# Performance work log

Measured on AMD Instinct MI355X. Metric: run time of the kernel, lower is better.

## Reference

```python
import jax, jax.numpy as jnp
import numpy as np

N_NODES = 50000
N_EDGES = 400000
D = 64        # hidden_features
H_NE = 16     # hidden_ne_features
L = 4         # num_layers
EPS = 1e-5


def _ln(z, g, b):
    # layer norm over feature dim
    mu = jnp.mean(z, axis=-1, keepdims=True)
    var = jnp.var(z, axis=-1, keepdims=True)
    return (z - mu) * jax.lax.rsqrt(var + EPS) * g + b


def setup_inputs() -> dict:
    key = jax.random.key(0)
    ks = iter(jax.random.split(key, 64))
    def rn(shape, s=0.05):
        return jax.random.normal(next(ks), shape, dtype=jnp.float32) * s
    inp = {
        "x": rn((N_NODES, 2), 1.0),
        "e": rn((N_EDGES, 2), 1.0),
        "src": jax.random.randint(next(ks), (N_EDGES,), 0, N_NODES, dtype=jnp.int32),
        "dst": jax.random.randint(next(ks), (N_EDGES,), 0, N_NODES, dtype=jnp.int32),
        # node / edge encoders (2-layer MLPs)
        "ne_W1": rn((2, H_NE)), "ne_b1": jnp.zeros((H_NE,), jnp.float32),
        "ne_W2": rn((H_NE, D)), "ne_b2": jnp.zeros((D,), jnp.float32),
        "ee_W1": rn((2, H_NE)), "ee_b1": jnp.zeros((H_NE,), jnp.float32),
        "ee_W2": rn((H_NE, D)), "ee_b2": jnp.zeros((D,), jnp.float32),
        # stacked per-layer GatedGCN weights
        "A1": rn((L, D, D)), "bA1": jnp.zeros((L, D), jnp.float32),
        "A2": rn((L, D, D)), "bA2": jnp.zeros((L, D), jnp.float32),
        "A3": rn((L, D, D)), "bA3": jnp.zeros((L, D), jnp.float32),
        "B1": rn((L, D, D)), "bB1": jnp.zeros((L, D), jnp.float32),
        "B2": rn((L, D, D)), "bB2": jnp.zeros((L, D), jnp.float32),
        "B3": rn((L, D, D)), "bB3": jnp.zeros((L, D), jnp.float32),
        "ge": jnp.ones((L, D), jnp.float32), "be": jnp.zeros((L, D), jnp.float32),
        "gh": jnp.ones((L, D), jnp.float32), "bh": jnp.zeros((L, D), jnp.float32),
        # score predictor
        "pW1": rn((3 * D, D)), "pb1": jnp.zeros((D,), jnp.float32),
        "pW2": rn((D, 1)), "pb2": jnp.zeros((1,), jnp.float32),
    }
    return inp


def _forward(x, e, src, dst,
             ne_W1, ne_b1, ne_W2, ne_b2,
             ee_W1, ee_b1, ee_W2, ee_b2,
             A1, bA1, A2, bA2, A3, bA3,
             B1, bB1, B2, bB2, B3, bB3,
             ge, be, gh, bh,
             pW1, pb1, pW2, pb2):
    # encoders
    x = jax.nn.relu(x @ ne_W1 + ne_b1) @ ne_W2 + ne_b2      # [N, D]
    e = jax.nn.relu(e @ ee_W1 + ee_b1) @ ee_W2 + ee_b2      # [E, D]

    params = {"A1": A1, "bA1": bA1, "A2": A2, "bA2": bA2,
              "A3": A3, "bA3": bA3, "B1": B1, "bB1": bB1,
              "B2": B2, "bB2": bB2, "B3": B3, "bB3": bB3,
              "ge": ge, "be": be, "gh": gh, "bh": bh}

    def layer(carry, p):
        x, e = carry
        # edge update: e_ij += ReLU(LN(B1 h_i + B2 h_j + B3 e_ij))
        e_hat = (x[src] @ p["B1"] + p["bB1"]
                 + x[dst] @ p["B2"] + p["bB2"]
                 + e @ p["B3"] + p["bB3"])                  # [E, D]
        e = e + jax.nn.relu(_ln(e_hat, p["ge"], p["be"]))
        sigma = jax.nn.sigmoid(e)                             # gates [E, D]
        # directed aggregation: forward (src->dst) and backward (dst->src)
        a2 = x @ p["A2"] + p["bA2"]
        a3 = x @ p["A3"] + p["bA3"]
        m_f = jax.ops.segment_sum(sigma * a2[src], dst, num_segments=N_NODES)
        d_f = jax.ops.segment_sum(sigma, dst, num_segments=N_NODES)
        m_b = jax.ops.segment_sum(sigma * a3[dst], src, num_segments=N_NODES)
        d_b = jax.ops.segment_sum(sigma, src, num_segments=N_NODES)
        h = (x @ p["A1"] + p["bA1"]
             + m_f / (d_f + EPS) + m_b / (d_b + EPS))        # [N, D]
        x = x + jax.nn.relu(_ln(h, p["gh"], p["bh"]))
        return (x, e), None

    (x, e), _ = jax.lax.scan(layer, (x, e), params)

    # score predictor: MLP over cat(x_src, x_dst, e)
    z = jnp.concatenate([x[src], x[dst], e], axis=-1)        # [E, 3D]
    return jax.nn.relu(z @ pW1 + pb1) @ pW2 + pb2            # [E, 1]


def reference(x, e, src, dst,
              ne_W1, ne_b1, ne_W2, ne_b2,
              ee_W1, ee_b1, ee_W2, ee_b2,
              A1, bA1, A2, bA2, A3, bA3,
              B1, bB1, B2, bB2, B3, bB3,
              ge, be, gh, bh,
              pW1, pb1, pW2, pb2):
    return _forward(x, e, src, dst,
                    ne_W1, ne_b1, ne_W2, ne_b2,
                    ee_W1, ee_b1, ee_W2, ee_b2,
                    A1, bA1, A2, bA2, A3, bA3,
                    B1, bB1, B2, bB2, B3, bB3,
                    ge, be, gh, bh,
                    pW1, pb1, pW2, pb2)
```

## Files before the change

kernel.cpp:

```cpp
#include <hip/hip_runtime.h>

#define N_NODES 50000
#define N_EDGES 400000
#define EPSV 1e-5f

__global__ __launch_bounds__(256) void encode_kernel(
    const float* __restrict__ in2, const float* __restrict__ W1,
    const float* __restrict__ b1, const float* __restrict__ W2,
    const float* __restrict__ b2, float* __restrict__ out, int nrows)
{
  int t = blockIdx.x * 256 + threadIdx.x;
  int row = t >> 4;
  int d0 = t & 15;
  if (row >= nrows) return;
  float x0 = in2[row * 2 + 0], x1 = in2[row * 2 + 1];
  float h[16];
#pragma unroll
  for (int j = 0; j < 16; ++j)
    h[j] = fmaxf(fmaf(x0, W1[j], fmaf(x1, W1[16 + j], b1[j])), 0.f);
#pragma unroll
  for (int q = 0; q < 4; ++q) {
    int d = d0 + q * 16;
    float a = b2[d];
#pragma unroll
    for (int j = 0; j < 16; ++j) a = fmaf(h[j], W2[j * 64 + d], a);
    out[(size_t)row * 64 + d] = a;
  }
}

__global__ __launch_bounds__(256) void hist_kernel(
    const int* __restrict__ src, const int* __restrict__ dst,
    int* __restrict__ cnt_f, int* __restrict__ cnt_b)
{
  int t = blockIdx.x * 256 + threadIdx.x;
  if (t >= N_EDGES) return;
  atomicAdd(&cnt_f[dst[t]], 1);
  atomicAdd(&cnt_b[src[t]], 1);
}

__global__ __launch_bounds__(1024) void scan_kernel(
    const int* __restrict__ cnt_f, const int* __restrict__ cnt_b,
    int* __restrict__ off_f, int* __restrict__ off_b,
    int* __restrict__ cur_f, int* __restrict__ cur_b)
{
  __shared__ int sh[1024];
  const int n = N_NODES;
  const int SEG = (n + 1023) / 1024;
  const int* cnt = blockIdx.x ? cnt_b : cnt_f;
  int* off = blockIdx.x ? off_b : off_f;
  int* cur = blockIdx.x ? cur_b : cur_f;
  int t = threadIdx.x;
  int base = t * SEG;
  int s = 0;
  for (int i = 0; i < SEG; ++i) {
    int idx = base + i;
    if (idx < n) s += cnt[idx];
  }
  sh[t] = s;
  __syncthreads();
  for (int o = 1; o < 1024; o <<= 1) {
    int v = sh[t];
    int u = (t >= o) ? sh[t - o] : 0;
    __syncthreads();
    sh[t] = v + u;
    __syncthreads();
  }
  int run = (t > 0) ? sh[t - 1] : 0;
  for (int i = 0; i < SEG; ++i) {
    int idx = base + i;
    if (idx < n) {
      off[idx] = run;
      cur[idx] = run;
      run += cnt[idx];
    }
  }
  if (t == 1023) off[n] = sh[1023];
}

__global__ __launch_bounds__(256) void fill_kernel(
    const int* __restrict__ src, const int* __restrict__ dst,
    int* __restrict__ cur_f, int* __restrict__ cur_b,
    int2* __restrict__ csr_f, int2* __restrict__ csr_b)
{
  int t = blockIdx.x * 256 + threadIdx.x;
  if (t >= N_EDGES) return;
  int dv = dst[t], sv = src[t];
  int p = atomicAdd(&cur_f[dv], 1);
  csr_f[p] = make_int2(t, sv);
  int q = atomicAdd(&cur_b[sv], 1);
  csr_b[q] = make_int2(t, dv);
}

__global__ __launch_bounds__(256) void sort_kernel(
    const int* __restrict__ off_f, const int* __restrict__ off_b,
    int2* __restrict__ csr_f, int2* __restrict__ csr_b)
{
  int t = blockIdx.x * 256 + threadIdx.x;
  int n;
  int2* csr;
  const int* off;
  if (t < N_NODES) { n = t; csr = csr_f; off = off_f; }
  else if (t < 2 * N_NODES) { n = t - N_NODES; csr = csr_b; off = off_b; }
  else return;
  int b = off[n], e = off[n + 1];
  for (int i = b + 1; i < e; ++i) {
    int2 key = csr[i];
    int j = i - 1;
    while (j >= b && csr[j].x > key.x) { csr[j + 1] = csr[j]; --j; }
    csr[j + 1] = key;
  }
}


__global__ __launch_bounds__(256, 3) void node_gemm_kernel(
    const float* __restrict__ X,
    const float* __restrict__ A1, const float* __restrict__ A2,
    const float* __restrict__ A3, const float* __restrict__ B1,
    const float* __restrict__ B2,
    const float* __restrict__ bA1, const float* __restrict__ bA2,
    const float* __restrict__ bA3, const float* __restrict__ bB1,
    const float* __restrict__ bB2,
    float* __restrict__ NA, int l)
{
  __shared__ float ett[4][64 * 36];
  const int NT = 1563;
  int wid = threadIdx.x >> 6;
  int lane = threadIdx.x & 63;
  int wf = blockIdx.x * 4 + wid;
  if (wf >= 5 * NT) return;
  int m = wf / NT;
  int t = wf - m * NT;
  int row0 = t * 32;
  int r8 = lane & 7, c8 = lane >> 3;
  int col = 8 * c8;
  float* tl = ett[wid];
#pragma unroll
  for (int rb = 0; rb < 8; ++rb) {
    int r = row0 + 4 * rb;
    float v0 = (r + 0 < N_NODES) ? X[(size_t)(r + 0) * 64 + lane] : 0.f;
    float v1 = (r + 1 < N_NODES) ? X[(size_t)(r + 1) * 64 + lane] : 0.f;
    float v2 = (r + 2 < N_NODES) ? X[(size_t)(r + 2) * 64 + lane] : 0.f;
    float v3 = (r + 3 < N_NODES) ? X[(size_t)(r + 3) * 64 + lane] : 0.f;
    *reinterpret_cast<float4*>(&tl[lane * 36 + 4 * rb]) =
        make_float4(v0, v1, v2, v3);
  }
  const float* W;
  const float* bb;
  if (m == 0) { W = A1; bb = bA1; }
  else if (m == 1) { W = A2; bb = bA2; }
  else if (m == 2) { W = A3; bb = bA3; }
  else if (m == 3) { W = B1; bb = bB1; }
  else { W = B2; bb = bB2; }
  W += l * 64 * 64;
  float acc[4][8];
#pragma unroll
  for (int i = 0; i < 4; ++i)
#pragma unroll
    for (int j = 0; j < 8; ++j) acc[i][j] = 0.f;
#pragma unroll 8
  for (int k = 0; k < 64; ++k) {
    float4 er = *reinterpret_cast<const float4*>(&tl[k * 36 + 4 * r8]);
    float4 w0 = *reinterpret_cast<const float4*>(&W[k * 64 + col]);
    float4 w1 = *reinterpret_cast<const float4*>(&W[k * 64 + col + 4]);
    float ev[4] = {er.x, er.y, er.z, er.w};
    float wv[8] = {w0.x, w0.y, w0.z, w0.w, w1.x, w1.y, w1.z, w1.w};
#pragma unroll
    for (int i = 0; i < 4; ++i)
#pragma unroll
      for (int j = 0; j < 8; ++j) acc[i][j] = fmaf(ev[i], wv[j], acc[i][j]);
  }
  float4 b0 = *reinterpret_cast<const float4*>(&bb[l * 64 + col]);
  float4 b1 = *reinterpret_cast<const float4*>(&bb[l * 64 + col + 4]);
  float* out = NA + (size_t)m * N_NODES * 64;
#pragma unroll
  for (int i = 0; i < 4; ++i) {
    int row = row0 + 4 * r8 + i;
    if (row < N_NODES) {
      *reinterpret_cast<float4*>(&out[(size_t)row * 64 + col]) =
          make_float4(acc[i][0] + b0.x, acc[i][1] + b0.y, acc[i][2] + b0.z,
                      acc[i][3] + b0.w);
      *reinterpret_cast<float4*>(&out[(size_t)row * 64 + col + 4]) =
          make_float4(acc[i][4] + b1.x, acc[i][5] + b1.y, acc[i][6] + b1.z,
                      acc[i][7] + b1.w);
    }
  }
}

__global__ __launch_bounds__(256, 3) void edge_update_kernel(
    const float* __restrict__ NA,
    const float* __restrict__ B3, const float* __restrict__ bB3,
    const float* __restrict__ ge, const float* __restrict__ be,
    const int* __restrict__ src, const int* __restrict__ dst,
    float* __restrict__ E64, int l)
{
  __shared__ float ett[4][64 * 36];
  int wid = threadIdx.x >> 6;
  int lane = threadIdx.x & 63;
  int tile = blockIdx.x * 4 + wid;
  int e0 = tile * 32;
  int r8 = lane & 7, c8 = lane >> 3;
  int col = 8 * c8;
  float* tl = ett[wid];
#pragma unroll
  for (int rb = 0; rb < 8; ++rb) {
    int r = e0 + 4 * rb;
    float v0 = E64[(size_t)(r + 0) * 64 + lane];
    float v1 = E64[(size_t)(r + 1) * 64 + lane];
    float v2 = E64[(size_t)(r + 2) * 64 + lane];
    float v3 = E64[(size_t)(r + 3) * 64 + lane];
    *reinterpret_cast<float4*>(&tl[lane * 36 + 4 * rb]) =
        make_float4(v0, v1, v2, v3);
  }
  const float* W = B3 + l * 64 * 64;
  float acc[4][8];
#pragma unroll
  for (int i = 0; i < 4; ++i)
#pragma unroll
    for (int j = 0; j < 8; ++j) acc[i][j] = 0.f;
#pragma unroll 8
  for (int k = 0; k < 64; ++k) {
    float4 er = *reinterpret_cast<const float4*>(&tl[k * 36 + 4 * r8]);
    float4 w0 = *reinterpret_cast<const float4*>(&W[k * 64 + col]);
    float4 w1 = *reinterpret_cast<const float4*>(&W[k * 64 + col + 4]);
    float ev[4] = {er.x, er.y, er.z, er.w};
    float wv[8] = {w0.x, w0.y, w0.z, w0.w, w1.x, w1.y, w1.z, w1.w};
#pragma unroll
    for (int i = 0; i < 4; ++i)
#pragma unroll
      for (int j = 0; j < 8; ++j) acc[i][j] = fmaf(ev[i], wv[j], acc[i][j]);
  }
  const float* b1x = NA + (size_t)3 * N_NODES * 64;
  const float* b2x = NA + (size_t)4 * N_NODES * 64;
  float4 t0, t1;
  t0 = *reinterpret_cast<const float4*>(&bB3[l * 64 + col]);
  t1 = *reinterpret_cast<const float4*>(&bB3[l * 64 + col + 4]);
  float bbv[8] = {t0.x, t0.y, t0.z, t0.w, t1.x, t1.y, t1.z, t1.w};
  t0 = *reinterpret_cast<const float4*>(&ge[l * 64 + col]);
  t1 = *reinterpret_cast<const float4*>(&ge[l * 64 + col + 4]);
  float gev[8] = {t0.x, t0.y, t0.z, t0.w, t1.x, t1.y, t1.z, t1.w};
  t0 = *reinterpret_cast<const float4*>(&be[l * 64 + col]);
  t1 = *reinterpret_cast<const float4*>(&be[l * 64 + col + 4]);
  float bev[8] = {t0.x, t0.y, t0.z, t0.w, t1.x, t1.y, t1.z, t1.w};
#pragma unroll
  for (int i = 0; i < 4; ++i) {
    int row = e0 + 4 * r8 + i;
    int sv = src[row], dv = dst[row];
    float4 g0 = *reinterpret_cast<const float4*>(&b1x[(size_t)sv * 64 + col]);
    float4 g1 = *reinterpret_cast<const float4*>(&b1x[(size_t)sv * 64 + col + 4]);
    float4 h0 = *reinterpret_cast<const float4*>(&b2x[(size_t)dv * 64 + col]);
    float4 h1 = *reinterpret_cast<const float4*>(&b2x[(size_t)dv * 64 + col + 4]);
    float4 o0 = *reinterpret_cast<const float4*>(&E64[(size_t)row * 64 + col]);
    float4 o1 = *reinterpret_cast<const float4*>(&E64[(size_t)row * 64 + col + 4]);
    float g1v[8] = {g0.x, g0.y, g0.z, g0.w, g1.x, g1.y, g1.z, g1.w};
    float g2v[8] = {h0.x, h0.y, h0.z, h0.w, h1.x, h1.y, h1.z, h1.w};
    float eov[8] = {o0.x, o0.y, o0.z, o0.w, o1.x, o1.y, o1.z, o1.w};
    float z[8];
    float s1 = 0.f, s2 = 0.f;
#pragma unroll
    for (int j = 0; j < 8; ++j) {
      z[j] = acc[i][j] + bbv[j] + g1v[j] + g2v[j];
      s1 += z[j];
      s2 = fmaf(z[j], z[j], s2);
    }
    s1 += __shfl_xor(s1, 8, 64);  s2 += __shfl_xor(s2, 8, 64);
    s1 += __shfl_xor(s1, 16, 64); s2 += __shfl_xor(s2, 16, 64);
    s1 += __shfl_xor(s1, 32, 64); s2 += __shfl_xor(s2, 32, 64);
    float mean = s1 * (1.f / 64.f);
    float var = fmaxf(s2 * (1.f / 64.f) - mean * mean, 0.f);
    float rstd = rsqrtf(var + EPSV);
    float o[8];
#pragma unroll
    for (int j = 0; j < 8; ++j)
      o[j] = eov[j] + fmaxf(fmaf((z[j] - mean) * rstd, gev[j], bev[j]), 0.f);
    *reinterpret_cast<float4*>(&E64[(size_t)row * 64 + col]) =
        make_float4(o[0], o[1], o[2], o[3]);
    *reinterpret_cast<float4*>(&E64[(size_t)row * 64 + col + 4]) =
        make_float4(o[4], o[5], o[6], o[7]);
  }
}

__global__ __launch_bounds__(256) void aggregate_kernel(
    const float* __restrict__ NA, const float* __restrict__ E64,
    const int* __restrict__ off_f, const int* __restrict__ off_b,
    const int2* __restrict__ csr_f, const int2* __restrict__ csr_b,
    const float* __restrict__ gh, const float* __restrict__ bh,
    float* __restrict__ X, int l)
{
  int wave = threadIdx.x >> 6;
  int lane = threadIdx.x & 63;
  int n = blockIdx.x * 4 + wave;
  if (n >= N_NODES) return;
  const float* A1x = NA;
  const float* A2x = NA + (size_t)N_NODES * 64;
  const float* A3x = NA + (size_t)2 * N_NODES * 64;
  float xo = X[(size_t)n * 64 + lane];
  float a1v = A1x[(size_t)n * 64 + lane];
  float ghv = gh[l * 64 + lane];
  float bhv = bh[l * 64 + lane];
  int pf = off_f[n], pfe = off_f[n + 1];
  int pb = off_b[n], pbe = off_b[n + 1];
  float mf = 0.f, df = 0.f, mb = 0.f, db = 0.f;
  bool hf = pf < pfe, hb = pb < pbe;
  float evf = 0.f, avf = 0.f, evb = 0.f, avb = 0.f;
  if (hf) {
    int2 c = csr_f[pf];
    evf = E64[(size_t)c.x * 64 + lane];
    avf = A2x[(size_t)c.y * 64 + lane];
  }
  if (hb) {
    int2 c = csr_b[pb];
    evb = E64[(size_t)c.x * 64 + lane];
    avb = A3x[(size_t)c.y * 64 + lane];
  }
  while (hf || hb) {
    bool nf = (pf + 1) < pfe;
    bool nb = (pb + 1) < pbe;
    float evf2 = 0.f, avf2 = 0.f, evb2 = 0.f, avb2 = 0.f;
    if (nf) {
      int2 c = csr_f[pf + 1];
      evf2 = E64[(size_t)c.x * 64 + lane];
      avf2 = A2x[(size_t)c.y * 64 + lane];
    }
    if (nb) {
      int2 c = csr_b[pb + 1];
      evb2 = E64[(size_t)c.x * 64 + lane];
      avb2 = A3x[(size_t)c.y * 64 + lane];
    }
    if (hf) {
      float sg = __builtin_amdgcn_rcpf(1.f + __expf(-evf));
      mf = fmaf(sg, avf, mf);
      df += sg;
      ++pf;
      evf = evf2;
      avf = avf2;
      hf = nf;
    }
    if (hb) {
      float sg = __builtin_amdgcn_rcpf(1.f + __expf(-evb));
      mb = fmaf(sg, avb, mb);
      db += sg;
      ++pb;
      evb = evb2;
      avb = avb2;
      hb = nb;
    }
  }
  float h = a1v + mf * __builtin_amdgcn_rcpf(df + EPSV) +
            mb * __builtin_amdgcn_rcpf(db + EPSV);
  float s1 = h, s2 = h * h;
#pragma unroll
  for (int m = 1; m < 64; m <<= 1) {
    s1 += __shfl_xor(s1, m, 64);
    s2 += __shfl_xor(s2, m, 64);
  }
  float mean = s1 * (1.f / 64.f);
  float var = fmaxf(s2 * (1.f / 64.f) - mean * mean, 0.f);
  float rstd = rsqrtf(var + EPSV);
  X[(size_t)n * 64 + lane] =
      xo + fmaxf(fmaf((h - mean) * rstd, ghv, bhv), 0.f);
}

__global__ __launch_bounds__(256, 3) void pred_node_kernel(
    const float* __restrict__ X, const float* __restrict__ pW1,
    float* __restrict__ U, float* __restrict__ V)
{
  __shared__ float ett[4][64 * 36];
  const int NT = 1563;
  int wid = threadIdx.x >> 6;
  int lane = threadIdx.x & 63;
  int wf = blockIdx.x * 4 + wid;
  if (wf >= 2 * NT) return;
  int m = wf / NT;
  int t = wf - m * NT;
  int row0 = t * 32;
  int r8 = lane & 7, c8 = lane >> 3;
  int col = 8 * c8;
  float* tl = ett[wid];
#pragma unroll
  for (int rb = 0; rb < 8; ++rb) {
    int r = row0 + 4 * rb;
    float v0 = (r + 0 < N_NODES) ? X[(size_t)(r + 0) * 64 + lane] : 0.f;
    float v1 = (r + 1 < N_NODES) ? X[(size_t)(r + 1) * 64 + lane] : 0.f;
    float v2 = (r + 2 < N_NODES) ? X[(size_t)(r + 2) * 64 + lane] : 0.f;
    float v3 = (r + 3 < N_NODES) ? X[(size_t)(r + 3) * 64 + lane] : 0.f;
    *reinterpret_cast<float4*>(&tl[lane * 36 + 4 * rb]) =
        make_float4(v0, v1, v2, v3);
  }
  const float* W = pW1 + (size_t)m * 64 * 64;
  float acc[4][8];
#pragma unroll
  for (int i = 0; i < 4; ++i)
#pragma unroll
    for (int j = 0; j < 8; ++j) acc[i][j] = 0.f;
#pragma unroll 8
  for (int k = 0; k < 64; ++k) {
    float4 er = *reinterpret_cast<const float4*>(&tl[k * 36 + 4 * r8]);
    float4 w0 = *reinterpret_cast<const float4*>(&W[k * 64 + col]);
    float4 w1 = *reinterpret_cast<const float4*>(&W[k * 64 + col + 4]);
    float ev[4] = {er.x, er.y, er.z, er.w};
    float wv[8] = {w0.x, w0.y, w0.z, w0.w, w1.x, w1.y, w1.z, w1.w};
#pragma unroll
    for (int i = 0; i < 4; ++i)
#pragma unroll
      for (int j = 0; j < 8; ++j) acc[i][j] = fmaf(ev[i], wv[j], acc[i][j]);
  }
  float* out = m ? V : U;
#pragma unroll
  for (int i = 0; i < 4; ++i) {
    int row = row0 + 4 * r8 + i;
    if (row < N_NODES) {
      *reinterpret_cast<float4*>(&out[(size_t)row * 64 + col]) =
          make_float4(acc[i][0], acc[i][1], acc[i][2], acc[i][3]);
      *reinterpret_cast<float4*>(&out[(size_t)row * 64 + col + 4]) =
          make_float4(acc[i][4], acc[i][5], acc[i][6], acc[i][7]);
    }
  }
}

__global__ __launch_bounds__(256, 3) void pred_edge_kernel(
    const float* __restrict__ U, const float* __restrict__ V,
    const float* __restrict__ E64,
    const int* __restrict__ src, const int* __restrict__ dst,
    const float* __restrict__ pW1, const float* __restrict__ pb1,
    const float* __restrict__ pW2, const float* __restrict__ pb2,
    float* __restrict__ out)
{
  __shared__ float ett[4][64 * 36];
  int wid = threadIdx.x >> 6;
  int lane = threadIdx.x & 63;
  int tile = blockIdx.x * 4 + wid;
  int e0 = tile * 32;
  int r8 = lane & 7, c8 = lane >> 3;
  int col = 8 * c8;
  float* tl = ett[wid];
#pragma unroll
  for (int rb = 0; rb < 8; ++rb) {
    int r = e0 + 4 * rb;
    float v0 = E64[(size_t)(r + 0) * 64 + lane];
    float v1 = E64[(size_t)(r + 1) * 64 + lane];
    float v2 = E64[(size_t)(r + 2) * 64 + lane];
    float v3 = E64[(size_t)(r + 3) * 64 + lane];
    *reinterpret_cast<float4*>(&tl[lane * 36 + 4 * rb]) =
        make_float4(v0, v1, v2, v3);
  }
  const float* W = pW1 + (size_t)128 * 64;
  float acc[4][8];
#pragma unroll
  for (int i = 0; i < 4; ++i)
#pragma unroll
    for (int j = 0; j < 8; ++j) acc[i][j] = 0.f;
#pragma unroll 8
  for (int k = 0; k < 64; ++k) {
    float4 er = *reinterpret_cast<const float4*>(&tl[k * 36 + 4 * r8]);
    float4 w0 = *reinterpret_cast<const float4*>(&W[k * 64 + col]);
    float4 w1 = *reinterpret_cast<const float4*>(&W[k * 64 + col + 4]);
    float ev[4] = {er.x, er.y, er.z, er.w};
    float wv[8] = {w0.x, w0.y, w0.z, w0.w, w1.x, w1.y, w1.z, w1.w};
#pragma unroll
    for (int i = 0; i < 4; ++i)
#pragma unroll
      for (int j = 0; j < 8; ++j) acc[i][j] = fmaf(ev[i], wv[j], acc[i][j]);
  }
  float4 t0, t1;
  t0 = *reinterpret_cast<const float4*>(&pb1[col]);
  t1 = *reinterpret_cast<const float4*>(&pb1[col + 4]);
  float pb1v[8] = {t0.x, t0.y, t0.z, t0.w, t1.x, t1.y, t1.z, t1.w};
  t0 = *reinterpret_cast<const float4*>(&pW2[col]);
  t1 = *reinterpret_cast<const float4*>(&pW2[col + 4]);
  float pw2v[8] = {t0.x, t0.y, t0.z, t0.w, t1.x, t1.y, t1.z, t1.w};
  float pb2v = pb2[0];
#pragma unroll
  for (int i = 0; i < 4; ++i) {
    int row = e0 + 4 * r8 + i;
    int sv = src[row], dv = dst[row];
    float4 g0 = *reinterpret_cast<const float4*>(&U[(size_t)sv * 64 + col]);
    float4 g1 = *reinterpret_cast<const float4*>(&U[(size_t)sv * 64 + col + 4]);
    float4 h0 = *reinterpret_cast<const float4*>(&V[(size_t)dv * 64 + col]);
    float4 h1 = *reinterpret_cast<const float4*>(&V[(size_t)dv * 64 + col + 4]);
    float g1v[8] = {g0.x, g0.y, g0.z, g0.w, g1.x, g1.y, g1.z, g1.w};
    float g2v[8] = {h0.x, h0.y, h0.z, h0.w, h1.x, h1.y, h1.z, h1.w};
    float hsum = 0.f;
#pragma unroll
    for (int j = 0; j < 8; ++j) {
      float z = acc[i][j] + pb1v[j] + g1v[j] + g2v[j];
      hsum = fmaf(fmaxf(z, 0.f), pw2v[j], hsum);
    }
    hsum += __shfl_xor(hsum, 8, 64);
    hsum += __shfl_xor(hsum, 16, 64);
    hsum += __shfl_xor(hsum, 32, 64);
    if (c8 == 0) out[row] = hsum + pb2v;
  }
}

extern "C" void kernel_launch(void* const* d_in, const int* in_sizes, int n_in,
                              void* d_out, int out_size, void* d_ws, size_t ws_size,
                              hipStream_t stream)
{
  const float* x = (const float*)d_in[0];
  const float* e = (const float*)d_in[1];
  const int* src = (const int*)d_in[2];
  const int* dst = (const int*)d_in[3];
  const float* neW1 = (const float*)d_in[4];
  const float* neb1 = (const float*)d_in[5];
  const float* neW2 = (const float*)d_in[6];
  const float* neb2 = (const float*)d_in[7];
  const float* eeW1 = (const float*)d_in[8];
  const float* eeb1 = (const float*)d_in[9];
  const float* eeW2 = (const float*)d_in[10];
  const float* eeb2 = (const float*)d_in[11];
  const float* A1 = (const float*)d_in[12];
  const float* bA1 = (const float*)d_in[13];
  const float* A2 = (const float*)d_in[14];
  const float* bA2 = (const float*)d_in[15];
  const float* A3 = (const float*)d_in[16];
  const float* bA3 = (const float*)d_in[17];
  const float* B1 = (const float*)d_in[18];
  const float* bB1 = (const float*)d_in[19];
  const float* B2 = (const float*)d_in[20];
  const float* bB2 = (const float*)d_in[21];
  const float* B3 = (const float*)d_in[22];
  const float* bB3 = (const float*)d_in[23];
  const float* ge = (const float*)d_in[24];
  const float* be = (const float*)d_in[25];
  const float* gh = (const float*)d_in[26];
  const float* bh = (const float*)d_in[27];
  const float* pW1 = (const float*)d_in[28];
  const float* pb1 = (const float*)d_in[29];
  const float* pW2 = (const float*)d_in[30];
  const float* pb2 = (const float*)d_in[31];

  char* ws = (char*)d_ws;
  float* X = (float*)ws;      ws += (size_t)N_NODES * 64 * 4;
  float* NA = (float*)ws;     ws += (size_t)5 * N_NODES * 64 * 4;
  float* E64 = (float*)ws;    ws += (size_t)N_EDGES * 64 * 4;
  int* cnt_f = (int*)ws;      ws += (size_t)N_NODES * 4;
  int* cnt_b = (int*)ws;      ws += (size_t)N_NODES * 4;
  int* off_f = (int*)ws;      ws += (size_t)(N_NODES + 1) * 4;
  int* off_b = (int*)ws;      ws += (size_t)(N_NODES + 1) * 4;
  int* cur_f = (int*)ws;      ws += (size_t)N_NODES * 4;
  int* cur_b = (int*)ws;      ws += (size_t)N_NODES * 4;
  int2* csr_f = (int2*)ws;    ws += (size_t)N_EDGES * 8;
  int2* csr_b = (int2*)ws;    ws += (size_t)N_EDGES * 8;
  float* U = NA + (size_t)3 * N_NODES * 64;
  float* V = NA + (size_t)4 * N_NODES * 64;

  encode_kernel<<<(N_NODES * 16 + 255) / 256, 256, 0, stream>>>(
      x, neW1, neb1, neW2, neb2, X, N_NODES);
  encode_kernel<<<(N_EDGES * 16 + 255) / 256, 256, 0, stream>>>(
      e, eeW1, eeb1, eeW2, eeb2, E64, N_EDGES);

  hipMemsetAsync(cnt_f, 0, (size_t)2 * N_NODES * 4, stream);
  hist_kernel<<<(N_EDGES + 255) / 256, 256, 0, stream>>>(src, dst, cnt_f, cnt_b);
  scan_kernel<<<2, 1024, 0, stream>>>(cnt_f, cnt_b, off_f, off_b, cur_f, cur_b);
  fill_kernel<<<(N_EDGES + 255) / 256, 256, 0, stream>>>(src, dst, cur_f, cur_b,
                                                         csr_f, csr_b);
  sort_kernel<<<(2 * N_NODES + 255) / 256, 256, 0, stream>>>(off_f, off_b, csr_f,
                                                             csr_b);

  const int NGB = (5 * 1563 + 3) / 4;
  const int PNB = (2 * 1563 + 3) / 4;
  for (int l = 0; l < 4; ++l) {
    node_gemm_kernel<<<NGB, 256, 0, stream>>>(
        X, A1, A2, A3, B1, B2, bA1, bA2, bA3, bB1, bB2, NA, l);
    edge_update_kernel<<<N_EDGES / 128, 256, 0, stream>>>(NA, B3, bB3, ge, be,
                                                          src, dst, E64, l);
    aggregate_kernel<<<(N_NODES + 3) / 4, 256, 0, stream>>>(
        NA, E64, off_f, off_b, csr_f, csr_b, gh, bh, X, l);
  }

  pred_node_kernel<<<PNB, 256, 0, stream>>>(X, pW1, U, V);
  pred_edge_kernel<<<N_EDGES / 128, 256, 0, stream>>>(U, V, E64, src, dst, pW1,
                                                      pb1, pW2, pb2,
                                                      (float*)d_out);
}
```

Baseline: 1.411 ms.

## Replace two-block prefix scan with three-phase multi-block scan

The CSR offset scan previously ran on only 2 blocks, each thread serially summing ~49 strided counts, so most of the GPU sat idle. It is now split into three kernels: a per-1024-chunk block scan across 98 blocks, a tiny serial scan of the block sums, and a per-element add pass. This spreads the work across many CUs and makes the loads coalesced. In exchange it adds two extra launches and a scratch buffer for partial sums.

```diff
diff --git a/kernel.cpp b/kernel.cpp
--- a/kernel.cpp
+++ b/kernel.cpp
@@ -3,6 +3,8 @@
 #define N_NODES 50000
 #define N_EDGES 400000
 #define EPSV 1e-5f
+#define SCAN_BLK 49
+#define SCAN_PAD (49 * 1024)
 
 __global__ __launch_bounds__(256) void encode_kernel(
     const float* __restrict__ in2, const float* __restrict__ W1,
@@ -38,43 +40,59 @@
   atomicAdd(&cnt_b[src[t]], 1);
 }
 
-__global__ __launch_bounds__(1024) void scan_kernel(
+__global__ __launch_bounds__(1024) void scanA_kernel(
     const int* __restrict__ cnt_f, const int* __restrict__ cnt_b,
+    int* __restrict__ part, int* __restrict__ bsum)
+{
+  int dir = blockIdx.x / SCAN_BLK;
+  int blk = blockIdx.x % SCAN_BLK;
+  const int* cnt = dir ? cnt_b : cnt_f;
+  int t = threadIdx.x;
+  int idx = blk * 1024 + t;
+  int v = (idx < N_NODES) ? cnt[idx] : 0;
+  __shared__ int sh[1024];
+  sh[t] = v;
+  __syncthreads();
+  for (int o = 1; o < 1024; o <<= 1) {
+    int u = (t >= o) ? sh[t - o] : 0;
+    __syncthreads();
+    sh[t] += u;
+    __syncthreads();
+  }
+  part[dir * SCAN_PAD + idx] = sh[t] - v;
+  if (t == 1023) bsum[dir * SCAN_BLK + blk] = sh[1023];
+}
+
+__global__ __launch_bounds__(64) void scanB_kernel(
+    int* __restrict__ bsum, int* __restrict__ off_f, int* __restrict__ off_b)
+{
+  int t = threadIdx.x;
+  if (t < 2) {
+    int* b = bsum + t * SCAN_BLK;
+    int run = 0;
+    for (int i = 0; i < SCAN_BLK; ++i) {
+      int v = b[i];
+      b[i] = run;
+      run += v;
+    }
+    if (t == 0) off_f[N_NODES] = run;
+    else off_b[N_NODES] = run;
+  }
+}
+
+__global__ __launch_bounds__(1024) void scanC_kernel(
+    const int* __restrict__ part, const int* __restrict__ bsum,
     int* __restrict__ off_f, int* __restrict__ off_b,
     int* __restrict__ cur_f, int* __restrict__ cur_b)
 {
-  __shared__ int sh[1024];
-  const int n = N_NODES;
-  const int SEG = (n + 1023) / 1024;
-  const int* cnt = blockIdx.x ? cnt_b : cnt_f;
-  int* off = blockIdx.x ? off_b : off_f;
-  int* cur = blockIdx.x ? cur_b : cur_f;
+  int dir = blockIdx.x / SCAN_BLK;
+  int blk = blockIdx.x % SCAN_BLK;
   int t = threadIdx.x;
-  int base = t * SEG;
-  int s = 0;
-  for (int i = 0; i < SEG; ++i) {
-    int idx = base + i;
-    if (idx < n) s += cnt[idx];
-  }
-  sh[t] = s;
-  __syncthreads();
-  for (int o = 1; o < 1024; o <<= 1) {
-    int v = sh[t];
-    int u = (t >= o) ? sh[t - o] : 0;
-    __syncthreads();
-    sh[t] = v + u;
-    __syncthreads();
-  }
-  int run = (t > 0) ? sh[t - 1] : 0;
-  for (int i = 0; i < SEG; ++i) {
-    int idx = base + i;
-    if (idx < n) {
-      off[idx] = run;
-      cur[idx] = run;
-      run += cnt[idx];
-    }
-  }
-  if (t == 1023) off[n] = sh[1023];
+  int idx = blk * 1024 + t;
+  if (idx >= N_NODES) return;
+  int v = part[dir * SCAN_PAD + idx] + bsum[dir * SCAN_BLK + blk];
+  if (dir == 0) { off_f[idx] = v; cur_f[idx] = v; }
+  else { off_b[idx] = v; cur_b[idx] = v; }
 }
 
 __global__ __launch_bounds__(256) void fill_kernel(
@@ -541,6 +559,8 @@
   int* cur_b = (int*)ws;      ws += (size_t)N_NODES * 4;
   int2* csr_f = (int2*)ws;    ws += (size_t)N_EDGES * 8;
   int2* csr_b = (int2*)ws;    ws += (size_t)N_EDGES * 8;
+  int* part = (int*)ws;       ws += (size_t)2 * SCAN_PAD * 4;
+  int* bsum = (int*)ws;       ws += (size_t)2 * SCAN_BLK * 4;
   float* U = NA + (size_t)3 * N_NODES * 64;
   float* V = NA + (size_t)4 * N_NODES * 64;
 
@@ -551,7 +571,10 @@
 
   hipMemsetAsync(cnt_f, 0, (size_t)2 * N_NODES * 4, stream);
   hist_kernel<<<(N_EDGES + 255) / 256, 256, 0, stream>>>(src, dst, cnt_f, cnt_b);
-  scan_kernel<<<2, 1024, 0, stream>>>(cnt_f, cnt_b, off_f, off_b, cur_f, cur_b);
+  scanA_kernel<<<2 * SCAN_BLK, 1024, 0, stream>>>(cnt_f, cnt_b, part, bsum);
+  scanB_kernel<<<1, 64, 0, stream>>>(bsum, off_f, off_b);
+  scanC_kernel<<<2 * SCAN_BLK, 1024, 0, stream>>>(part, bsum, off_f, off_b,
+                                                  cur_f, cur_b);
   fill_kernel<<<(N_EDGES + 255) / 256, 256, 0, stream>>>(src, dst, cur_f, cur_b,
                                                          csr_f, csr_b);
   sort_kernel<<<(2 * N_NODES + 255) / 256, 256, 0, stream>>>(off_f, off_b, csr_f,
```

After: 1.293 ms. 8.3% less time.
